# Kernel optimization log

Measured on AMD Instinct MI355X. Metric: run time of the kernel, lower is better.

## Reference

```python
import jax, jax.numpy as jnp
import numpy as np

N_ATOMS = 50000
N_EDGES = 800000
N_ATOM_BASIS = 128
N_FILTERS = 128
N_GAUSS = 64
CUTOFF = 5.0


def shifted_softplus(x):
    return jax.nn.softplus(x) - jnp.log(2.0)


def setup_inputs() -> dict:
    key = jax.random.key(0)
    ks = jax.random.split(key, 9)
    r = jax.random.normal(ks[0], (N_ATOMS, N_ATOM_BASIS), dtype=jnp.float32)
    # per-edge distances in [0, cutoff)
    e = jax.random.uniform(ks[1], (N_EDGES, 1), dtype=jnp.float32) * CUTOFF
    a = jax.random.randint(ks[2], (N_EDGES, 2), 0, N_ATOMS)  # [dst, src] per edge
    Wf2 = jax.random.normal(ks[3], (N_GAUSS, N_FILTERS), dtype=jnp.float32) / np.sqrt(N_GAUSS)
    bf2 = jnp.zeros((N_FILTERS,), jnp.float32)
    Wa = jax.random.normal(ks[4], (N_ATOM_BASIS, N_FILTERS), dtype=jnp.float32) / np.sqrt(N_ATOM_BASIS)
    W1 = jax.random.normal(ks[5], (N_FILTERS, N_ATOM_BASIS), dtype=jnp.float32) / np.sqrt(N_FILTERS)
    b1 = jnp.zeros((N_ATOM_BASIS,), jnp.float32)
    W2 = jax.random.normal(ks[6], (N_ATOM_BASIS, N_ATOM_BASIS), dtype=jnp.float32) / np.sqrt(N_ATOM_BASIS)
    b2 = jnp.zeros((N_ATOM_BASIS,), jnp.float32)
    return {"r": r, "e": e, "Wf2": Wf2, "bf2": bf2, "Wa": Wa,
            "W1": W1, "b1": b1, "W2": W2, "b2": b2, "a": a}


def reference(r, e, Wf2, bf2, Wa, W1, b1, W2, b2, a):
    # Gaussian smearing of per-edge distances: [E,1] -> [E,G]
    offsets = jnp.linspace(0.0, CUTOFF, N_GAUSS, dtype=jnp.float32)
    width = offsets[1] - offsets[0]
    coeff = -0.5 / (width * width)
    g = jnp.exp(coeff * jnp.square(e - offsets[None, :]))  # [E, G]
    # DistanceFilter2 (DistanceFilter1 output is overwritten in the original code)
    W = g @ Wf2 + bf2                      # [E, F] per-edge filter
    rf = r @ Wa                            # [N, F] AtomFilter (no bias)
    y = rf[a[:, 1]] * W                    # gather src nodes, modulate by filter
    y = jax.ops.segment_sum(y, a[:, 0], num_segments=N_ATOMS)  # scatter-add to dst
    y = shifted_softplus(y @ W1 + b1)      # Dense1
    y = y @ W2 + b2                        # Dense2 (no activation)
    return y
```

## Files before the change

### kernel.cpp

```cpp
#include <hip/hip_runtime.h>
#include <hip/hip_bf16.h>
#include <math.h>

#define NA 50000
#define NE 800000
#define WPB 4
#define NTILE 782
#define EGRID 2048
#define NWAVES (EGRID * WPB)
#define SCAT_BLKS 1024
#define RF_BLKS 782
#define TAB_BLKS 256
#define NTAB 16384
#define BCAP 64

typedef float f32x4 __attribute__((ext_vector_type(4)));
typedef __bf16 bf16x8 __attribute__((ext_vector_type(8)));

__device__ __forceinline__ float ssp(float x) {
    float z  = __expf(-fabsf(x));
    float lp = __logf(1.0f + z);
    return fmaxf(x, 0.0f) + lp - 0.69314718f;
}

__device__ __forceinline__ uint32_t pkbf2(float a, float b) {
    union { __bf16 h[2]; uint32_t u; } x;
    x.h[0] = (__bf16)a; x.h[1] = (__bf16)b;
    return x.u;
}

__global__ __launch_bounds__(256) void pack_weights(const float* __restrict__ Wa,
                                                    const float* __restrict__ W1,
                                                    const float* __restrict__ W2,
                                                    const float* __restrict__ Wf2,
                                                    __bf16* __restrict__ pWaH, __bf16* __restrict__ pWaL,
                                                    __bf16* __restrict__ pW1H, __bf16* __restrict__ pW1L,
                                                    __bf16* __restrict__ pW2H, __bf16* __restrict__ pW2L,
                                                    __bf16* __restrict__ pWf,
                                                    int* __restrict__ cursor) {
    const int t = blockIdx.x * 256 + threadIdx.x;
    const int stride = gridDim.x * 256;
    for (int i = t; i < 16384; i += stride) {
        int k = i >> 7, n = i & 127;
        int addr = n * 128 + (((k >> 3) ^ (n & 15)) << 3) + (k & 7);
        float v; __bf16 h;
        v = Wa[i]; h = (__bf16)v; pWaH[addr] = h; pWaL[addr] = (__bf16)(v - (float)h);
        v = W1[i]; h = (__bf16)v; pW1H[addr] = h; pW1L[addr] = (__bf16)(v - (float)h);
        v = W2[i]; h = (__bf16)v; pW2H[addr] = h; pW2L[addr] = (__bf16)(v - (float)h);
    }
    for (int i = t; i < 8192; i += stride) {
        int k = i >> 7, n = i & 127;
        int addr = n * 64 + (((k >> 3) ^ (n & 7)) << 3) + (k & 7);
        pWf[addr] = (__bf16)Wf2[i];
    }
    for (int i = t; i < NA; i += stride) cursor[i] = i * BCAP;
}

__device__ __forceinline__ void rf_gemm_packed(const float* __restrict__ A,
                                               const __bf16* __restrict__ pWh,
                                               const __bf16* __restrict__ pWl,
                                               void* __restrict__ C, int M,
                                               int blk, int gridn,
                                               __bf16* sWhi, __bf16* sWlo) {
    const int tid = threadIdx.x;
    {
        const uint4* ph = (const uint4*)pWh;
        const uint4* pl = (const uint4*)pWl;
        uint4* dh = (uint4*)sWhi;
        uint4* dl = (uint4*)sWlo;
        for (int i = tid; i < 2048; i += 256) { dh[i] = ph[i]; dl[i] = pl[i]; }
    }
    __syncthreads();

    const int lane = tid & 63, w = tid >> 6;
    const int lrow = lane & 15, lgrp = lane >> 4;

    for (int base = blk * 64; base < M; base += gridn * 64) {
        const int row  = base + w * 16 + lrow;
        const int rowc = row < M ? row : M - 1;

        f32x4 acc[8];
        #pragma unroll
        for (int nt = 0; nt < 8; ++nt) acc[nt] = (f32x4){0.f, 0.f, 0.f, 0.f};

        #pragma unroll
        for (int ks = 0; ks < 4; ++ks) {
            int k0 = ks * 32 + lgrp * 8;
            float4 f0 = *(const float4*)&A[(size_t)rowc * 128 + k0];
            float4 f1 = *(const float4*)&A[(size_t)rowc * 128 + k0 + 4];
            float av[8] = {f0.x, f0.y, f0.z, f0.w, f1.x, f1.y, f1.z, f1.w};
            bf16x8 ah, al;
            #pragma unroll
            for (int j = 0; j < 8; ++j) {
                __bf16 h = (__bf16)av[j];
                ah[j] = h;
                al[j] = (__bf16)(av[j] - (float)h);
            }
            #pragma unroll
            for (int nt = 0; nt < 8; ++nt) {
                int n = nt * 16 + lrow;
                int addr = n * 128 + (((ks * 4 + lgrp) ^ (n & 15)) << 3);
                bf16x8 bh = *(const bf16x8*)&sWhi[addr];
                bf16x8 bl = *(const bf16x8*)&sWlo[addr];
                acc[nt] = __builtin_amdgcn_mfma_f32_16x16x32_bf16(ah, bh, acc[nt], 0, 0, 0);
                acc[nt] = __builtin_amdgcn_mfma_f32_16x16x32_bf16(ah, bl, acc[nt], 0, 0, 0);
                acc[nt] = __builtin_amdgcn_mfma_f32_16x16x32_bf16(al, bh, acc[nt], 0, 0, 0);
            }
        }

        const int orow = base + w * 16 + lgrp * 4;
        #pragma unroll
        for (int r = 0; r < 4; ++r) {
            if (orow + r < M) {
                #pragma unroll
                for (int nt = 0; nt < 8; ++nt) {
                    ((__hip_bfloat16*)C)[(size_t)(orow + r) * 128 + nt * 16 + lrow] =
                        __float2bfloat16(acc[nt][r]);
                }
            }
        }
    }
}

__device__ __forceinline__ void tab_build(const __bf16* __restrict__ pWf,
                                          const float* __restrict__ bf2,
                                          __hip_bfloat16* __restrict__ wtab,
                                          int blk, __bf16* sWf) {
    const int tid = threadIdx.x;
    {
        const uint4* p = (const uint4*)pWf;
        uint4* d = (uint4*)sWf;
        for (int i = tid; i < 1024; i += 256) d[i] = p[i];
    }
    __syncthreads();

    const int lane = tid & 63, w = tid >> 6;
    const int lrow = lane & 15, lgrp = lane >> 4;

    float bv[8];
    #pragma unroll
    for (int nt = 0; nt < 8; ++nt) bv[nt] = bf2[nt * 16 + lrow];

    const float coeff = -0.5f * (63.0f / 5.0f) * (63.0f / 5.0f);
    const int row = blk * 64 + w * 16 + lrow;
    const float ev = ((float)row * 4.0f + 1.5f) * (1.0f / 13107.0f);

    bf16x8 ah[2];
    #pragma unroll
    for (int ks = 0; ks < 2; ++ks) {
        #pragma unroll
        for (int j = 0; j < 8; ++j) {
            int k = ks * 32 + lgrp * 8 + j;
            float dd = ev - (5.0f / 63.0f) * (float)k;
            ah[ks][j] = (__bf16)__expf(coeff * dd * dd);
        }
    }

    f32x4 c[8];
    #pragma unroll
    for (int nt = 0; nt < 8; ++nt) c[nt] = (f32x4){0.f, 0.f, 0.f, 0.f};
    #pragma unroll
    for (int ks = 0; ks < 2; ++ks) {
        #pragma unroll
        for (int nt = 0; nt < 8; ++nt) {
            int n = nt * 16 + lrow;
            int addr = n * 64 + (((ks * 4 + lgrp) ^ (n & 7)) << 3);
            bf16x8 bh = *(const bf16x8*)&sWf[addr];
            c[nt] = __builtin_amdgcn_mfma_f32_16x16x32_bf16(ah[ks], bh, c[nt], 0, 0, 0);
        }
    }

    const int orow = blk * 64 + w * 16 + lgrp * 4;
    #pragma unroll
    for (int r = 0; r < 4; ++r) {
        #pragma unroll
        for (int nt = 0; nt < 8; ++nt) {
            wtab[(size_t)(orow + r) * 128 + nt * 16 + lrow] =
                __float2bfloat16(c[nt][r] + bv[nt]);
        }
    }
}

__global__ __launch_bounds__(256) void front_fused(const int* __restrict__ a,
                                                   const float* __restrict__ e,
                                                   int* __restrict__ cursor,
                                                   uint32_t* __restrict__ bucket,
                                                   const float* __restrict__ r,
                                                   const __bf16* __restrict__ pWaH,
                                                   const __bf16* __restrict__ pWaL,
                                                   void* __restrict__ rfb,
                                                   const __bf16* __restrict__ pWf,
                                                   const float* __restrict__ bf2,
                                                   __hip_bfloat16* __restrict__ wtab) {
    __shared__ __bf16 sWhi[128 * 128];
    __shared__ __bf16 sWlo[128 * 128];
    if (blockIdx.x < SCAT_BLKS) {
        for (int i = blockIdx.x * 256 + threadIdx.x; i < NE; i += SCAT_BLKS * 256) {
            int2 dp = ((const int2*)a)[i];
            int pos = atomicAdd(&cursor[dp.x], 1);
            uint32_t eq = (uint32_t)(e[i] * 13107.0f + 0.5f);
            if (pos < dp.x * BCAP + BCAP)
                bucket[pos] = (eq << 16) | (uint32_t)dp.y;
        }
    } else if (blockIdx.x < SCAT_BLKS + RF_BLKS) {
        rf_gemm_packed(r, pWaH, pWaL, rfb, NA, blockIdx.x - SCAT_BLKS,
                       RF_BLKS, sWhi, sWlo);
    } else {
        tab_build(pWf, bf2, wtab, blockIdx.x - SCAT_BLKS - RF_BLKS, sWhi);
    }
}

__global__ __launch_bounds__(256, 8) void edge_fused(const int* __restrict__ cursor,
                                                     const uint32_t* __restrict__ bucket,
                                                     const uint32_t* __restrict__ wtab,
                                                     const uint32_t* __restrict__ rfb,
                                                     uint32_t* __restrict__ segb) {
    __shared__ uint32_t su[WPB][BCAP];
    __shared__ int      scnt[WPB][8];

    const int tid  = threadIdx.x;
    const int lane = tid & 63, w = tid >> 6;

    const int wi      = blockIdx.x * WPB + w;
    const int d_start = (int)(((long long)wi * NA) / NWAVES);
    const int d_end   = (int)(((long long)(wi + 1) * NA) / NWAVES);
    const int dcount  = d_end - d_start;

    if (lane < dcount) {
        int c = cursor[d_start + lane] - (d_start + lane) * BCAP;
        scnt[w][lane] = (c < BCAP) ? c : BCAP;
    }
    __builtin_amdgcn_wave_barrier();

    uint32_t* su_w = su[w];

    for (int di = 0; di < dcount; ++di) {
        const int d   = d_start + di;
        const int cnt = scnt[w][di];

        su_w[lane] = bucket[(size_t)d * BCAP + lane];
        __builtin_amdgcn_wave_barrier();

        float racc0 = 0.0f, racc1 = 0.0f;
        for (int j0 = 0; j0 < cnt; j0 += 16) {
            uint32_t rw[16], tw[16];
            #pragma unroll
            for (int j = 0; j < 16; ++j) {
                int jj = (j0 + j < cnt) ? (j0 + j) : (cnt - 1);
                uint32_t u = su_w[jj];
                rw[j] = rfb[(size_t)(u & 0xFFFFu) * 64 + lane];
                tw[j] = wtab[(size_t)(u >> 18) * 64 + lane];
            }
            #pragma unroll
            for (int j = 0; j < 16; ++j) {
                if (j0 + j < cnt) {
                    racc0 = fmaf(__uint_as_float(rw[j] << 16),
                                 __uint_as_float(tw[j] << 16), racc0);
                    racc1 = fmaf(__uint_as_float(rw[j] & 0xFFFF0000u),
                                 __uint_as_float(tw[j] & 0xFFFF0000u), racc1);
                }
            }
        }
        segb[(size_t)d * 64 + lane] = pkbf2(racc0, racc1);
        __builtin_amdgcn_wave_barrier();
    }
}

__global__ __launch_bounds__(256) void dense1(const uint32_t* __restrict__ segb,
                                              const __bf16* __restrict__ pW1H,
                                              const __bf16* __restrict__ pW1L,
                                              const float* __restrict__ b1,
                                              void* __restrict__ y1b) {
    __shared__ __bf16 sWhi[128 * 128];
    __shared__ __bf16 sWlo[128 * 128];
    const int tid = threadIdx.x;
    {
        const uint4* ph = (const uint4*)pW1H;
        const uint4* pl = (const uint4*)pW1L;
        uint4* dh = (uint4*)sWhi;
        uint4* dl = (uint4*)sWlo;
        for (int i = tid; i < 2048; i += 256) { dh[i] = ph[i]; dl[i] = pl[i]; }
    }
    __syncthreads();

    const int lane = tid & 63, w = tid >> 6;
    const int lrow = lane & 15, lgrp = lane >> 4;
    const __bf16* seg = (const __bf16*)segb;

    float bv[8];
    #pragma unroll
    for (int nt = 0; nt < 8; ++nt) bv[nt] = b1[nt * 16 + lrow];

    const int base = blockIdx.x * 64;
    const int row  = base + w * 16 + lrow;
    const int rowc = row < NA ? row : NA - 1;

    f32x4 acc[8];
    #pragma unroll
    for (int nt = 0; nt < 8; ++nt) acc[nt] = (f32x4){0.f, 0.f, 0.f, 0.f};

    #pragma unroll
    for (int ks = 0; ks < 4; ++ks) {
        int k0 = ks * 32 + lgrp * 8;
        bf16x8 ya = *(const bf16x8*)&seg[(size_t)rowc * 128 + k0];
        #pragma unroll
        for (int nt = 0; nt < 8; ++nt) {
            int n = nt * 16 + lrow;
            int addr = n * 128 + (((ks * 4 + lgrp) ^ (n & 15)) << 3);
            bf16x8 bh = *(const bf16x8*)&sWhi[addr];
            bf16x8 bl = *(const bf16x8*)&sWlo[addr];
            acc[nt] = __builtin_amdgcn_mfma_f32_16x16x32_bf16(ya, bh, acc[nt], 0, 0, 0);
            acc[nt] = __builtin_amdgcn_mfma_f32_16x16x32_bf16(ya, bl, acc[nt], 0, 0, 0);
        }
    }

    const int orow = base + w * 16 + lgrp * 4;
    #pragma unroll
    for (int r = 0; r < 4; ++r) {
        if (orow + r < NA) {
            #pragma unroll
            for (int nt = 0; nt < 8; ++nt) {
                float v = ssp(acc[nt][r] + bv[nt]);
                ((__hip_bfloat16*)y1b)[(size_t)(orow + r) * 128 + nt * 16 + lrow] =
                    __float2bfloat16(v);
            }
        }
    }
}

__global__ __launch_bounds__(256) void dense2(const void* __restrict__ y1b,
                                              const __bf16* __restrict__ pW2H,
                                              const __bf16* __restrict__ pW2L,
                                              const float* __restrict__ b2,
                                              float* __restrict__ out) {
    __shared__ __bf16 sWhi[128 * 128];
    __shared__ __bf16 sWlo[128 * 128];
    const int tid = threadIdx.x;
    {
        const uint4* ph = (const uint4*)pW2H;
        const uint4* pl = (const uint4*)pW2L;
        uint4* dh = (uint4*)sWhi;
        uint4* dl = (uint4*)sWlo;
        for (int i = tid; i < 2048; i += 256) { dh[i] = ph[i]; dl[i] = pl[i]; }
    }
    __syncthreads();

    const int lane = tid & 63, w = tid >> 6;
    const int lrow = lane & 15, lgrp = lane >> 4;
    const __bf16* y1 = (const __bf16*)y1b;

    float bv[8];
    #pragma unroll
    for (int nt = 0; nt < 8; ++nt) bv[nt] = b2[nt * 16 + lrow];

    const int base = blockIdx.x * 64;
    const int row  = base + w * 16 + lrow;
    const int rowc = row < NA ? row : NA - 1;

    f32x4 acc[8];
    #pragma unroll
    for (int nt = 0; nt < 8; ++nt) acc[nt] = (f32x4){0.f, 0.f, 0.f, 0.f};

    #pragma unroll
    for (int ks = 0; ks < 4; ++ks) {
        int k0 = ks * 32 + lgrp * 8;
        bf16x8 ya = *(const bf16x8*)&y1[(size_t)rowc * 128 + k0];
        #pragma unroll
        for (int nt = 0; nt < 8; ++nt) {
            int n = nt * 16 + lrow;
            int addr = n * 128 + (((ks * 4 + lgrp) ^ (n & 15)) << 3);
            bf16x8 bh = *(const bf16x8*)&sWhi[addr];
            bf16x8 bl = *(const bf16x8*)&sWlo[addr];
            acc[nt] = __builtin_amdgcn_mfma_f32_16x16x32_bf16(ya, bh, acc[nt], 0, 0, 0);
            acc[nt] = __builtin_amdgcn_mfma_f32_16x16x32_bf16(ya, bl, acc[nt], 0, 0, 0);
        }
    }

    const int orow = base + w * 16 + lgrp * 4;
    #pragma unroll
    for (int r = 0; r < 4; ++r) {
        if (orow + r < NA) {
            #pragma unroll
            for (int nt = 0; nt < 8; ++nt) {
                out[(size_t)(orow + r) * 128 + nt * 16 + lrow] = acc[nt][r] + bv[nt];
            }
        }
    }
}

extern "C" void kernel_launch(void* const* d_in, const int* in_sizes, int n_in,
                              void* d_out, int out_size, void* d_ws, size_t ws_size,
                              hipStream_t stream) {
    const float* r   = (const float*)d_in[0];
    const float* e   = (const float*)d_in[1];
    const float* Wf2 = (const float*)d_in[2];
    const float* bf2 = (const float*)d_in[3];
    const float* Wa  = (const float*)d_in[4];
    const float* W1  = (const float*)d_in[5];
    const float* b1  = (const float*)d_in[6];
    const float* W2  = (const float*)d_in[7];
    const float* b2  = (const float*)d_in[8];
    const int*   a   = (const int*)d_in[9];

    float* out = (float*)d_out;

    uint32_t* rfb    = (uint32_t*)d_ws;
    uint32_t* y1b    = (uint32_t*)d_ws + 3200000;
    uint32_t* segb   = (uint32_t*)d_ws + 6400000;
    int*      cursor = (int*)d_ws + 9600000;
    __bf16*   pWaH   = (__bf16*)((int*)d_ws + 9650048);
    __bf16*   pWaL   = pWaH + 16384;
    __bf16*   pW1H   = pWaL + 16384;
    __bf16*   pW1L   = pW1H + 16384;
    __bf16*   pW2H   = pW1L + 16384;
    __bf16*   pW2L   = pW2H + 16384;
    __bf16*   pWf    = pW2L + 16384;

    __hip_bfloat16* wtab   = (__hip_bfloat16*)d_out;
    uint32_t*       bucket = (uint32_t*)d_out + 1310720;

    pack_weights<<<64, 256, 0, stream>>>(Wa, W1, W2, Wf2,
                                         pWaH, pWaL, pW1H, pW1L, pW2H, pW2L,
                                         pWf, cursor);

    front_fused<<<SCAT_BLKS + RF_BLKS + TAB_BLKS, 256, 0, stream>>>(
        a, e, cursor, bucket, r, pWaH, pWaL, rfb, pWf, bf2, wtab);

    edge_fused<<<EGRID, 256, 0, stream>>>(cursor, bucket, (const uint32_t*)wtab,
                                          rfb, segb);

    dense1<<<NTILE, 256, 0, stream>>>(segb, pW1H, pW1L, b1, y1b);
    dense2<<<NTILE, 256, 0, stream>>>(y1b, pW2H, pW2L, b2, out);
}
```

Before: 157.3 us.

## Read packed weight fragments directly from global memory instead of LDS staging

Weights are repacked into a fragment-major layout so each lane's 8-element MFMA B operand is one contiguous 16-byte global load, coalesced across the wavefront. Every GEMM kernel (rf, table build, dense1, dense2) drops its 64KB shared-memory staging copy and the block barrier. This frees LDS, which can raise occupancy, and removes per-block weight copy overhead. In exchange, weight reads now depend on L1/L2 cache hits in the inner MFMA loop instead of LDS.

```diff
diff --git a/kernel.cpp b/kernel.cpp
--- a/kernel.cpp
+++ b/kernel.cpp
@@ -42,7 +42,9 @@
     const int stride = gridDim.x * 256;
     for (int i = t; i < 16384; i += stride) {
         int k = i >> 7, n = i & 127;
-        int addr = n * 128 + (((k >> 3) ^ (n & 15)) << 3) + (k & 7);
+        int ks = k >> 5, km = k & 31, lg = km >> 3, j = km & 7;
+        int nt = n >> 4, lr = n & 15;
+        int addr = ((((ks * 8 + nt) * 4 + lg) * 16 + lr) << 3) + j;
         float v; __bf16 h;
         v = Wa[i]; h = (__bf16)v; pWaH[addr] = h; pWaL[addr] = (__bf16)(v - (float)h);
         v = W1[i]; h = (__bf16)v; pW1H[addr] = h; pW1L[addr] = (__bf16)(v - (float)h);
@@ -50,28 +52,20 @@
     }
     for (int i = t; i < 8192; i += stride) {
         int k = i >> 7, n = i & 127;
-        int addr = n * 64 + (((k >> 3) ^ (n & 7)) << 3) + (k & 7);
+        int ks = k >> 5, km = k & 31, lg = km >> 3, j = km & 7;
+        int nt = n >> 4, lr = n & 15;
+        int addr = ((((ks * 8 + nt) * 4 + lg) * 16 + lr) << 3) + j;
         pWf[addr] = (__bf16)Wf2[i];
     }
     for (int i = t; i < NA; i += stride) cursor[i] = i * BCAP;
 }
 
-__device__ __forceinline__ void rf_gemm_packed(const float* __restrict__ A,
-                                               const __bf16* __restrict__ pWh,
-                                               const __bf16* __restrict__ pWl,
-                                               void* __restrict__ C, int M,
-                                               int blk, int gridn,
-                                               __bf16* sWhi, __bf16* sWlo) {
-    const int tid = threadIdx.x;
-    {
-        const uint4* ph = (const uint4*)pWh;
-        const uint4* pl = (const uint4*)pWl;
-        uint4* dh = (uint4*)sWhi;
-        uint4* dl = (uint4*)sWlo;
-        for (int i = tid; i < 2048; i += 256) { dh[i] = ph[i]; dl[i] = pl[i]; }
-    }
-    __syncthreads();
-
+__device__ __forceinline__ void rf_gemm_g(const float* __restrict__ A,
+                                          const __bf16* __restrict__ pWh,
+                                          const __bf16* __restrict__ pWl,
+                                          void* __restrict__ C, int M,
+                                          int blk, int gridn) {
+    const int tid  = threadIdx.x;
     const int lane = tid & 63, w = tid >> 6;
     const int lrow = lane & 15, lgrp = lane >> 4;
 
@@ -98,10 +92,9 @@
             }
             #pragma unroll
             for (int nt = 0; nt < 8; ++nt) {
-                int n = nt * 16 + lrow;
-                int addr = n * 128 + (((ks * 4 + lgrp) ^ (n & 15)) << 3);
-                bf16x8 bh = *(const bf16x8*)&sWhi[addr];
-                bf16x8 bl = *(const bf16x8*)&sWlo[addr];
+                const int goff = (((ks << 3) + nt) << 9) + (lane << 3);
+                bf16x8 bh = *(const bf16x8*)&pWh[goff];
+                bf16x8 bl = *(const bf16x8*)&pWl[goff];
                 acc[nt] = __builtin_amdgcn_mfma_f32_16x16x32_bf16(ah, bh, acc[nt], 0, 0, 0);
                 acc[nt] = __builtin_amdgcn_mfma_f32_16x16x32_bf16(ah, bl, acc[nt], 0, 0, 0);
                 acc[nt] = __builtin_amdgcn_mfma_f32_16x16x32_bf16(al, bh, acc[nt], 0, 0, 0);
@@ -125,15 +118,8 @@
 __device__ __forceinline__ void tab_build(const __bf16* __restrict__ pWf,
                                           const float* __restrict__ bf2,
                                           __hip_bfloat16* __restrict__ wtab,
-                                          int blk, __bf16* sWf) {
-    const int tid = threadIdx.x;
-    {
-        const uint4* p = (const uint4*)pWf;
-        uint4* d = (uint4*)sWf;
-        for (int i = tid; i < 1024; i += 256) d[i] = p[i];
-    }
-    __syncthreads();
-
+                                          int blk) {
+    const int tid  = threadIdx.x;
     const int lane = tid & 63, w = tid >> 6;
     const int lrow = lane & 15, lgrp = lane >> 4;
 
@@ -163,9 +149,7 @@
     for (int ks = 0; ks < 2; ++ks) {
         #pragma unroll
         for (int nt = 0; nt < 8; ++nt) {
-            int n = nt * 16 + lrow;
-            int addr = n * 64 + (((ks * 4 + lgrp) ^ (n & 7)) << 3);
-            bf16x8 bh = *(const bf16x8*)&sWf[addr];
+            bf16x8 bh = *(const bf16x8*)&pWf[(((ks << 3) + nt) << 9) + (lane << 3)];
             c[nt] = __builtin_amdgcn_mfma_f32_16x16x32_bf16(ah[ks], bh, c[nt], 0, 0, 0);
         }
     }
@@ -192,8 +176,6 @@
                                                    const __bf16* __restrict__ pWf,
                                                    const float* __restrict__ bf2,
                                                    __hip_bfloat16* __restrict__ wtab) {
-    __shared__ __bf16 sWhi[128 * 128];
-    __shared__ __bf16 sWlo[128 * 128];
     if (blockIdx.x < SCAT_BLKS) {
         for (int i = blockIdx.x * 256 + threadIdx.x; i < NE; i += SCAT_BLKS * 256) {
             int2 dp = ((const int2*)a)[i];
@@ -203,10 +185,9 @@
                 bucket[pos] = (eq << 16) | (uint32_t)dp.y;
         }
     } else if (blockIdx.x < SCAT_BLKS + RF_BLKS) {
-        rf_gemm_packed(r, pWaH, pWaL, rfb, NA, blockIdx.x - SCAT_BLKS,
-                       RF_BLKS, sWhi, sWlo);
+        rf_gemm_g(r, pWaH, pWaL, rfb, NA, blockIdx.x - SCAT_BLKS, RF_BLKS);
     } else {
-        tab_build(pWf, bf2, wtab, blockIdx.x - SCAT_BLKS - RF_BLKS, sWhi);
+        tab_build(pWf, bf2, wtab, blockIdx.x - SCAT_BLKS - RF_BLKS);
     }
 }
 
@@ -271,18 +252,7 @@
                                               const __bf16* __restrict__ pW1L,
                                               const float* __restrict__ b1,
                                               void* __restrict__ y1b) {
-    __shared__ __bf16 sWhi[128 * 128];
-    __shared__ __bf16 sWlo[128 * 128];
-    const int tid = threadIdx.x;
-    {
-        const uint4* ph = (const uint4*)pW1H;
-        const uint4* pl = (const uint4*)pW1L;
-        uint4* dh = (uint4*)sWhi;
-        uint4* dl = (uint4*)sWlo;
-        for (int i = tid; i < 2048; i += 256) { dh[i] = ph[i]; dl[i] = pl[i]; }
-    }
-    __syncthreads();
-
+    const int tid  = threadIdx.x;
     const int lane = tid & 63, w = tid >> 6;
     const int lrow = lane & 15, lgrp = lane >> 4;
     const __bf16* seg = (const __bf16*)segb;
@@ -305,10 +275,9 @@
         bf16x8 ya = *(const bf16x8*)&seg[(size_t)rowc * 128 + k0];
         #pragma unroll
         for (int nt = 0; nt < 8; ++nt) {
-            int n = nt * 16 + lrow;
-            int addr = n * 128 + (((ks * 4 + lgrp) ^ (n & 15)) << 3);
-            bf16x8 bh = *(const bf16x8*)&sWhi[addr];
-            bf16x8 bl = *(const bf16x8*)&sWlo[addr];
+            const int goff = (((ks << 3) + nt) << 9) + (lane << 3);
+            bf16x8 bh = *(const bf16x8*)&pW1H[goff];
+            bf16x8 bl = *(const bf16x8*)&pW1L[goff];
             acc[nt] = __builtin_amdgcn_mfma_f32_16x16x32_bf16(ya, bh, acc[nt], 0, 0, 0);
             acc[nt] = __builtin_amdgcn_mfma_f32_16x16x32_bf16(ya, bl, acc[nt], 0, 0, 0);
         }
@@ -333,18 +302,7 @@
                                               const __bf16* __restrict__ pW2L,
                                               const float* __restrict__ b2,
                                               float* __restrict__ out) {
-    __shared__ __bf16 sWhi[128 * 128];
-    __shared__ __bf16 sWlo[128 * 128];
-    const int tid = threadIdx.x;
-    {
-        const uint4* ph = (const uint4*)pW2H;
-        const uint4* pl = (const uint4*)pW2L;
-        uint4* dh = (uint4*)sWhi;
-        uint4* dl = (uint4*)sWlo;
-        for (int i = tid; i < 2048; i += 256) { dh[i] = ph[i]; dl[i] = pl[i]; }
-    }
-    __syncthreads();
-
+    const int tid  = threadIdx.x;
     const int lane = tid & 63, w = tid >> 6;
     const int lrow = lane & 15, lgrp = lane >> 4;
     const __bf16* y1 = (const __bf16*)y1b;
@@ -367,10 +325,9 @@
         bf16x8 ya = *(const bf16x8*)&y1[(size_t)rowc * 128 + k0];
         #pragma unroll
         for (int nt = 0; nt < 8; ++nt) {
-            int n = nt * 16 + lrow;
-            int addr = n * 128 + (((ks * 4 + lgrp) ^ (n & 15)) << 3);
-            bf16x8 bh = *(const bf16x8*)&sWhi[addr];
-            bf16x8 bl = *(const bf16x8*)&sWlo[addr];
+            const int goff = (((ks << 3) + nt) << 9) + (lane << 3);
+            bf16x8 bh = *(const bf16x8*)&pW2H[goff];
+            bf16x8 bl = *(const bf16x8*)&pW2L[goff];
             acc[nt] = __builtin_amdgcn_mfma_f32_16x16x32_bf16(ya, bh, acc[nt], 0, 0, 0);
             acc[nt] = __builtin_amdgcn_mfma_f32_16x16x32_bf16(ya, bl, acc[nt], 0, 0, 0);
         }
```

Result: slower. 160.9 us (+2.3%).
